# Kernel optimization log

Hardware: AMD Instinct MI355X
Metric: run time of the kernel (lower is better)

Reference implementation:

```python
import jax, jax.numpy as jnp
import numpy as np

NUM_HEADS = 16
LN_EPS = 1e-5


def setup_inputs() -> dict:
    key = jax.random.key(0)
    k1, k2, k3 = jax.random.split(key, 3)
    E = 1024
    B, S = 4, 2048
    return {
        "rotation_params": jax.random.normal(k1, (E, E), dtype=jnp.float32) * (E ** -0.5),
        "entangle_params": jax.random.normal(k2, (E, E), dtype=jnp.float32) * (E ** -0.5),
        "inputs": jax.random.normal(k3, (B, S, E), dtype=jnp.float32),
        "ln_weight": jnp.ones((E,), dtype=jnp.float32),
        "ln_bias": jnp.zeros((E,), dtype=jnp.float32),
    }


def reference(rotation_params, entangle_params, inputs, ln_weight, ln_bias):
    x = inputs  # (B, S, E)
    B, S, E = x.shape
    H = NUM_HEADS
    D = E // H
    scale = D ** -0.5

    q = jnp.einsum('bse,ef->bsf', x, rotation_params)
    k = jnp.einsum('bse,ef->bsf', x, entangle_params)
    v = x  # forward uses raw inputs as values

    # split heads: (B, H, S, D)
    q = q.reshape(B, S, H, D).transpose(0, 2, 1, 3)
    k = k.reshape(B, S, H, D).transpose(0, 2, 1, 3)
    v = v.reshape(B, S, H, D).transpose(0, 2, 1, 3)

    scores = jnp.einsum('bhsd,bhtd->bhst', q, k) * scale  # (B, H, S, S)
    attn = jax.nn.softmax(scores, axis=-1)
    context = jnp.einsum('bhst,bhtd->bhsd', attn, v)
    context = context.transpose(0, 2, 1, 3).reshape(B, S, E)

    # residual + LayerNorm
    y = context + x
    mu = jnp.mean(y, axis=-1, keepdims=True)
    var = jnp.mean(jnp.square(y - mu), axis=-1, keepdims=True)
    y = (y - mu) * jax.lax.rsqrt(var + LN_EPS)
    return y * ln_weight + ln_bias
```

## Files before the change

kernel.cpp:

```cpp
#include <hip/hip_runtime.h>
#include <hip/hip_bf16.h>

#define LOG2E 1.44269504088896340736f

typedef __attribute__((ext_vector_type(8)))  short  short8;
typedef __attribute__((ext_vector_type(2)))  float  f32x2;
typedef __attribute__((ext_vector_type(4)))  float  f32x4;
typedef __attribute__((ext_vector_type(16))) float  f32x16;

__device__ __forceinline__ unsigned short f2bf(float f) {
  unsigned u = __builtin_bit_cast(unsigned, f);
  return (unsigned short)((u + 0x8000u) >> 16);
}
__device__ __forceinline__ float bf2f(unsigned short u) {
  return __builtin_bit_cast(float, (unsigned)u << 16);
}
__device__ __forceinline__ f32x2 pkadd(f32x2 a, f32x2 b) {
  f32x2 r; asm("v_pk_add_f32 %0, %1, %2" : "=v"(r) : "v"(a), "v"(b)); return r;
}
__device__ __forceinline__ unsigned cvtpk2(float a, float b) {
  unsigned r; asm("v_cvt_pk_bf16_f32 %0, %1, %2" : "=v"(r) : "v"(a), "v"(b)); return r;
}
__device__ __forceinline__ float hexp2(float x) {
  float r; asm("v_exp_f32 %0, %1" : "=v"(r) : "v"(x)); return r;
}
__device__ __forceinline__ float m3(float a, float b, float c) {
  return fmaxf(fmaxf(a, b), c);
}
__device__ __forceinline__ void gl16(const void* g, void* l) {
  __builtin_amdgcn_global_load_lds(
      (const __attribute__((address_space(1))) void*)g,
      (__attribute__((address_space(3))) void*)l, 16, 0, 0);
}

__global__ __launch_bounds__(256) void prep_all(const float* __restrict__ R,
                                                const float* __restrict__ En,
                                                const float* __restrict__ x,
                                                unsigned short* __restrict__ Rt,
                                                unsigned short* __restrict__ Et,
                                                unsigned short* __restrict__ vt,
                                                unsigned short* __restrict__ xb) {
  int id = blockIdx.x;
  int tid = threadIdx.x;
  __shared__ unsigned short t[64][65];
  if (id < 2048) {
    int bh = id >> 5, st = id & 31;
    int b = bh >> 4, h = bh & 15;
    int s0 = st * 64;
#pragma unroll
    for (int i = 0; i < 4; i++) {
      int it = i * 256 + tid;
      int row = it >> 4, c4 = (it & 15) * 4;
      size_t goff = (size_t)(b * 2048 + s0 + row) * 1024 + h * 64 + c4;
      float4 v = *(const float4*)(x + goff);
      ushort4 o;
      o.x = f2bf(v.x); o.y = f2bf(v.y); o.z = f2bf(v.z); o.w = f2bf(v.w);
      *(ushort4*)(xb + goff) = o;
      t[c4 + 0][row] = o.x; t[c4 + 1][row] = o.y;
      t[c4 + 2][row] = o.z; t[c4 + 3][row] = o.w;
    }
    __syncthreads();
    int r = tid >> 2, c4 = (tid & 3) * 16;
    short8 o0, o1;
#pragma unroll
    for (int j = 0; j < 8; j++) {
      o0[j] = (short)t[r][c4 + j];
      o1[j] = (short)t[r][c4 + 8 + j];
    }
    *(short8*)(vt + (size_t)(bh * 64 + r) * 2048 + s0 + c4) = o0;
    *(short8*)(vt + (size_t)(bh * 64 + r) * 2048 + s0 + c4 + 8) = o1;
  } else {
    int z = id - 2048;
    const float* src = (z >= 256) ? En : R;
    unsigned short* dst = (z >= 256) ? Et : Rt;
    int rem = z & 255;
    int e0 = (rem >> 4) * 64, f0 = (rem & 15) * 64;
    int r = tid >> 2, c4 = (tid & 3) * 16;
#pragma unroll
    for (int j = 0; j < 16; j += 4) {
      float4 v = *(const float4*)(src + (size_t)(e0 + r) * 1024 + f0 + c4 + j);
      t[c4 + j + 0][r] = f2bf(v.x);
      t[c4 + j + 1][r] = f2bf(v.y);
      t[c4 + j + 2][r] = f2bf(v.z);
      t[c4 + j + 3][r] = f2bf(v.w);
    }
    __syncthreads();
    short8 o0, o1;
#pragma unroll
    for (int j = 0; j < 8; j++) {
      o0[j] = (short)t[r][c4 + j];
      o1[j] = (short)t[r][c4 + 8 + j];
    }
    *(short8*)(dst + (size_t)(f0 + r) * 1024 + e0 + c4) = o0;
    *(short8*)(dst + (size_t)(f0 + r) * 1024 + e0 + c4 + 8) = o1;
  }
}

__global__ __launch_bounds__(512, 2) void gemm8(const unsigned short* __restrict__ A,
                                                const unsigned short* __restrict__ Bw,
                                                unsigned short* __restrict__ qb,
                                                unsigned short* __restrict__ kb,
                                                float qs) {
  int m0 = blockIdx.x * 256;
  int by = blockIdx.y;
  int n0 = by * 256;
  int tid = threadIdx.x;
  int w = tid >> 6, l = tid & 63;
  int wr = w >> 2, wc = w & 3;
  int l15 = l & 15, lq = l >> 4;

  __shared__ unsigned short As[2][2][128 * 64];
  __shared__ unsigned short Bs[2][2][128 * 64];

  f32x4 acc[8][4] = {};

  int key = (l15 & 7) << 4;
  const char* pA[2];
  const char* pB[2];
#pragma unroll
  for (int kk = 0; kk < 2; kk++) {
    pA[kk] = (const char*)As + wr * 16384 + l15 * 128 + ((kk * 64 + lq * 16) ^ key);
    pB[kk] = (const char*)Bs + (wc >> 1) * 16384 + ((wc & 1) * 64 + l15) * 128 +
             ((kk * 64 + lq * 16) ^ key);
  }

#define SHALF(buf, kt, which)                                                 \
  do {                                                                        \
    const unsigned short* src_ = ((which) < 2)                                \
        ? (A  + (size_t)(m0 + ((which) & 1) * 128) * 1024)                    \
        : (Bw + (size_t)(n0 + ((which) & 1) * 128) * 1024);                   \
    char* dst_ = (char*)(((which) < 2) ? &As[buf][(which) & 1][0]             \
                                       : &Bs[buf][(which) & 1][0]);           \
    int k0_ = (kt) * 64;                                                      \
    _Pragma("unroll") for (int i_ = 0; i_ < 2; i_++) {                        \
      int flat_ = i_ * 512 + tid;                                             \
      int row_ = flat_ >> 3, ch_ = flat_ & 7;                                 \
      gl16(src_ + (size_t)row_ * 1024 + k0_ + ((ch_ ^ (row_ & 7)) << 3),      \
           dst_ + i_ * 8192 + w * 1024);                                      \
    }                                                                         \
  } while (0)

#define BARX()                                                                \
  do {                                                                        \
    __builtin_amdgcn_sched_barrier(0);                                        \
    asm volatile("" ::: "memory");                                            \
    __builtin_amdgcn_s_barrier();                                             \
    asm volatile("" ::: "memory");                                            \
    __builtin_amdgcn_sched_barrier(0);                                        \
  } while (0)

#define DSRD(buf, mq, nq)                                                     \
  short8 af[4][2]; short8 bfv[2][2];                                          \
  _Pragma("unroll") for (int mfq = 0; mfq < 4; mfq++)                         \
    _Pragma("unroll") for (int kk = 0; kk < 2; kk++)                          \
      af[mfq][kk] = *(const short8*)(pA[kk] + (buf) * 32768 + (mq) * 8192 +   \
                                     mfq * 2048);                             \
  _Pragma("unroll") for (int nfq = 0; nfq < 2; nfq++)                         \
    _Pragma("unroll") for (int kk = 0; kk < 2; kk++)                          \
      bfv[nfq][kk] = *(const short8*)(pB[kk] + (buf) * 32768 + (nq) * 4096 +  \
                                      nfq * 2048);

#define MM(mq, nq)                                                            \
  asm volatile("s_waitcnt lgkmcnt(0)" ::: "memory");                          \
  __builtin_amdgcn_sched_barrier(0);                                          \
  __builtin_amdgcn_s_setprio(1);                                              \
  _Pragma("unroll") for (int mfq = 0; mfq < 4; mfq++)                         \
    _Pragma("unroll") for (int nfq = 0; nfq < 2; nfq++)                       \
      _Pragma("unroll") for (int kk = 0; kk < 2; kk++)                        \
        acc[(mq) * 4 + mfq][(nq) * 2 + nfq] =                                 \
            __builtin_amdgcn_mfma_f32_16x16x32_bf16(                          \
                af[mfq][kk], bfv[nfq][kk],                                    \
                acc[(mq) * 4 + mfq][(nq) * 2 + nfq], 0, 0, 0);                \
  __builtin_amdgcn_s_setprio(0);

  SHALF(0, 0, 0); SHALF(0, 0, 1); SHALF(0, 0, 2); SHALF(0, 0, 3);
  asm volatile("s_waitcnt vmcnt(0)" ::: "memory");
  BARX();

  for (int kt = 0; kt < 16; kt++) {
    int buf = kt & 1, nb = buf ^ 1;
    {
      DSRD(buf, 0, 0);
      if (kt < 15) { SHALF(nb, kt + 1, 0); SHALF(nb, kt + 1, 1); }
      MM(0, 0);
      BARX();
    }
    {
      DSRD(buf, 0, 1);
      if (kt < 15) { SHALF(nb, kt + 1, 2); SHALF(nb, kt + 1, 3); }
      MM(0, 1);
      BARX();
    }
    {
      DSRD(buf, 1, 0);
      MM(1, 0);
      BARX();
    }
    {
      DSRD(buf, 1, 1);
      MM(1, 1);
      asm volatile("s_waitcnt vmcnt(0)" ::: "memory");
      BARX();
    }
  }
#undef SHALF
#undef DSRD
#undef MM
#undef BARX

  unsigned short* out = (by < 4) ? qb : kb;
  float scale = (by < 4) ? qs : 1.0f;
  int cb = (by & 3) * 256;
#pragma unroll
  for (int mf = 0; mf < 8; mf++)
#pragma unroll
    for (int nf = 0; nf < 4; nf++)
#pragma unroll
      for (int r = 0; r < 4; r++) {
        int grow = m0 + wr * 128 + mf * 16 + lq * 4 + r;
        int gcol = cb + wc * 64 + nf * 16 + l15;
        out[(size_t)grow * 1024 + gcol] = f2bf(acc[mf][nf][r] * scale);
      }
}

__global__ __launch_bounds__(256, 4) void attn_k(const unsigned short* __restrict__ Q,
                                                 const unsigned short* __restrict__ K,
                                                 const unsigned short* __restrict__ VT,
                                                 unsigned short* __restrict__ ctx) {
  int f = blockIdx.x;
  int bh = ((f >> 7) << 3) | (f & 7);
  int qt = (f >> 3) & 15;
  int b = bh >> 4, h = bh & 15;
  int q0 = qt * 128;
  int tid = threadIdx.x;
  int w = tid >> 6, l = tid & 63;
  int lh = l >> 5, l31 = l & 31;

  __shared__ unsigned short Kl[2 * 64 * 64];
  __shared__ unsigned short Vl[2 * 64 * 64];

  int qrow = q0 + w * 32 + l31;
  const unsigned short* qp = Q + (size_t)(b * 2048 + qrow) * 1024 + h * 64;
  short8 qf[4];
#pragma unroll
  for (int dk = 0; dk < 4; dk++) qf[dk] = *(const short8*)(qp + dk * 16 + lh * 8);

  int key = (l31 & 7) << 4;
  int koff[4], voff[4];
#pragma unroll
  for (int dk = 0; dk < 4; dk++) koff[dk] = l31 * 128 + ((dk * 32 + lh * 16) ^ key);
#pragma unroll
  for (int tf = 0; tf < 2; tf++)
#pragma unroll
    for (int kk = 0; kk < 2; kk++)
      voff[tf * 2 + kk] = l31 * 128 + ((tf * 64 + kk * 32 + lh * 16) ^ key);

  const char* KB = (const char*)Kl;
  const char* VB = (const char*)Vl;

  f32x16 cacc[2] = {};
  float mrun = -INFINITY, lsl = 0.f;

#define STAGE(buf, tt)                                                        \
  {                                                                           \
    _Pragma("unroll") for (int i_ = 0; i_ < 2; i_++) {                        \
      int row_ = i_ * 32 + (tid >> 3), ch_ = tid & 7;                         \
      gl16(K + (size_t)(b * 2048 + (tt) + row_) * 1024 + h * 64 +             \
               ((ch_ ^ (row_ & 7)) << 3),                                     \
           (char*)Kl + (buf) * 8192 + i_ * 4096 + w * 1024);                  \
      gl16(VT + (size_t)(bh * 64 + row_) * 2048 + (tt) +                      \
               ((ch_ ^ (row_ & 7)) << 3),                                     \
           (char*)Vl + (buf) * 8192 + i_ * 4096 + w * 1024);                  \
    }                                                                         \
  }

#define COMPUTE(IMM)                                                          \
  do {                                                                        \
    f32x16 sacc[2] = {};                                                      \
    __builtin_amdgcn_s_setprio(1);                                            \
    _Pragma("unroll") for (int tf = 0; tf < 2; tf++)                          \
      _Pragma("unroll") for (int dk = 0; dk < 4; dk++) {                      \
        short8 kf = *(const short8*)(KB + koff[dk] + (IMM) + tf * 4096);      \
        sacc[tf] = __builtin_amdgcn_mfma_f32_32x32x16_bf16(kf, qf[dk],        \
                                                           sacc[tf], 0, 0, 0);\
      }                                                                       \
    __builtin_amdgcn_s_setprio(0);                                            \
    float t16[16];                                                            \
    _Pragma("unroll") for (int j = 0; j < 16; j++)                            \
      t16[j] = fmaxf(sacc[0][j], sacc[1][j]);                                 \
    float t8[8];                                                              \
    _Pragma("unroll") for (int j = 0; j < 8; j++)                             \
      t8[j] = fmaxf(t16[j], t16[j + 8]);                                      \
    float lmax = m3(m3(t8[0], t8[1], t8[2]), m3(t8[3], t8[4], t8[5]),         \
                    fmaxf(t8[6], t8[7]));                                     \
    if (!__all(lmax <= mrun + 8.f)) {                                         \
      unsigned lu = __builtin_bit_cast(unsigned, lmax);                       \
      auto rr = __builtin_amdgcn_permlane32_swap(lu, lu, false, false);       \
      float pm = fmaxf(__builtin_bit_cast(float, rr[0]),                      \
                       __builtin_bit_cast(float, rr[1]));                     \
      float mnew = fmaxf(mrun, pm);                                           \
      float alpha = hexp2(mrun - mnew);                                       \
      mrun = mnew; lsl *= alpha;                                              \
      _Pragma("unroll") for (int r = 0; r < 16; r++) {                        \
        int rowq = (r & 3) + ((r >> 2) << 3) + (lh << 2);                     \
        float ar = __shfl(alpha, rowq, 64);                                   \
        cacc[0][r] *= ar; cacc[1][r] *= ar;                                   \
      }                                                                       \
    }                                                                         \
    f32x2 negm2; negm2[0] = -mrun; negm2[1] = -mrun;                          \
    f32x2 r2; r2[0] = 0.f; r2[1] = 0.f;                                       \
    _Pragma("unroll") for (int tf = 0; tf < 2; tf++) {                        \
      unsigned pw[8];                                                         \
      _Pragma("unroll") for (int j = 0; j < 8; j++) {                         \
        f32x2 s2; s2[0] = sacc[tf][2 * j]; s2[1] = sacc[tf][2 * j + 1];       \
        f32x2 d = pkadd(s2, negm2);                                           \
        float e0 = hexp2(d[0]), e1 = hexp2(d[1]);                             \
        f32x2 e2; e2[0] = e0; e2[1] = e1;                                     \
        r2 = pkadd(r2, e2);                                                   \
        pw[j] = cvtpk2(e0, e1);                                               \
      }                                                                       \
      short8 pa[2];                                                           \
      _Pragma("unroll") for (int kk = 0; kk < 2; kk++) {                      \
        auto r02 = __builtin_amdgcn_permlane32_swap(pw[kk * 4 + 0],           \
                                                    pw[kk * 4 + 2], false, false); \
        auto r13 = __builtin_amdgcn_permlane32_swap(pw[kk * 4 + 1],           \
                                                    pw[kk * 4 + 3], false, false); \
        union { unsigned u[4]; short8 s8; } wv;                               \
        wv.u[0] = r02[0]; wv.u[1] = r13[0];                                   \
        wv.u[2] = r02[1]; wv.u[3] = r13[1];                                   \
        pa[kk] = wv.s8;                                                       \
      }                                                                       \
      __builtin_amdgcn_s_setprio(1);                                          \
      _Pragma("unroll") for (int kk = 0; kk < 2; kk++)                        \
        _Pragma("unroll") for (int df = 0; df < 2; df++) {                    \
          short8 vf = *(const short8*)(VB + voff[tf * 2 + kk] + (IMM) +       \
                                       df * 4096);                            \
          cacc[df] = __builtin_amdgcn_mfma_f32_32x32x16_bf16(pa[kk], vf,      \
                                                             cacc[df], 0, 0, 0); \
        }                                                                     \
      __builtin_amdgcn_s_setprio(0);                                          \
    }                                                                         \
    lsl += r2[0] + r2[1];                                                     \
  } while (0)

  STAGE(0, 0);
  __syncthreads();

  for (int tc2 = 0; tc2 < 16; tc2++) {
    int t0 = tc2 * 128;
    STAGE(1, t0 + 64);
    COMPUTE(0);
    __syncthreads();
    if (tc2 < 15) STAGE(0, t0 + 128);
    COMPUTE(8192);
    __syncthreads();
  }
#undef STAGE
#undef COMPUTE

  {
    unsigned lu = __builtin_bit_cast(unsigned, lsl);
    auto rr = __builtin_amdgcn_permlane32_swap(lu, lu, false, false);
    lsl = __builtin_bit_cast(float, rr[0]) + __builtin_bit_cast(float, rr[1]);
  }
  float linv = 1.f / lsl;
#pragma unroll
  for (int r = 0; r < 16; r++) {
    int rowq = (r & 3) + ((r >> 2) << 3) + (lh << 2);
    float lr = __shfl(linv, rowq, 64);
    size_t base = (size_t)(b * 2048 + q0 + w * 32 + rowq) * 1024 + h * 64 + l31;
    ctx[base]      = f2bf(cacc[0][r] * lr);
    ctx[base + 32] = f2bf(cacc[1][r] * lr);
  }
}

__global__ __launch_bounds__(256) void ln_k(const unsigned short* __restrict__ ctx,
                                            const float* __restrict__ x,
                                            const float* __restrict__ wgt,
                                            const float* __restrict__ bgam,
                                            float* __restrict__ out) {
  int w = threadIdx.x >> 6, l = threadIdx.x & 63;
  size_t base = ((size_t)blockIdx.x * 4 + w) * 1024;
  float y[16];
  float s = 0.f, ss = 0.f;
#pragma unroll
  for (int j = 0; j < 4; j++) {
    int col = j * 256 + l * 4;
    ushort4 cu = *(const ushort4*)(ctx + base + col);
    float4 xv = *(const float4*)(x + base + col);
    float y0 = bf2f(cu.x) + xv.x, y1 = bf2f(cu.y) + xv.y;
    float y2 = bf2f(cu.z) + xv.z, y3 = bf2f(cu.w) + xv.w;
    y[4 * j + 0] = y0; y[4 * j + 1] = y1; y[4 * j + 2] = y2; y[4 * j + 3] = y3;
    s += (y0 + y1) + (y2 + y3);
    ss += (y0 * y0 + y1 * y1) + (y2 * y2 + y3 * y3);
  }
#pragma unroll
  for (int o = 32; o >= 1; o >>= 1) {
    s  += __shfl_xor(s, o, 64);
    ss += __shfl_xor(ss, o, 64);
  }
  float mu = s * (1.f / 1024.f);
  float var = ss * (1.f / 1024.f) - mu * mu;
  float rstd = rsqrtf(var + 1e-5f);
#pragma unroll
  for (int j = 0; j < 4; j++) {
    int col = j * 256 + l * 4;
    float4 wv = *(const float4*)(wgt + col);
    float4 bv = *(const float4*)(bgam + col);
    float4 o4;
    o4.x = (y[4 * j + 0] - mu) * rstd * wv.x + bv.x;
    o4.y = (y[4 * j + 1] - mu) * rstd * wv.y + bv.y;
    o4.z = (y[4 * j + 2] - mu) * rstd * wv.z + bv.z;
    o4.w = (y[4 * j + 3] - mu) * rstd * wv.w + bv.w;
    *(float4*)(out + base + col) = o4;
  }
}

extern "C" void kernel_launch(void* const* d_in, const int* in_sizes, int n_in,
                              void* d_out, int out_size, void* d_ws, size_t ws_size,
                              hipStream_t stream) {
  (void)in_sizes; (void)n_in; (void)out_size; (void)ws_size;
  const float* R  = (const float*)d_in[0];
  const float* En = (const float*)d_in[1];
  const float* x  = (const float*)d_in[2];
  const float* lw = (const float*)d_in[3];
  const float* lb = (const float*)d_in[4];
  float* out = (float*)d_out;

  char* ws = (char*)d_ws;
  unsigned short* xb  = (unsigned short*)(ws);
  unsigned short* qb  = (unsigned short*)(ws + (size_t)(16u << 20));
  unsigned short* kb  = (unsigned short*)(ws + (size_t)(32u << 20));
  unsigned short* vt  = (unsigned short*)(ws + (size_t)(48u << 20));
  unsigned short* ctx = (unsigned short*)(ws + (size_t)(64u << 20));
  unsigned short* rt  = (unsigned short*)(ws + (size_t)(96u << 20));
  unsigned short* et  = (unsigned short*)(ws + (size_t)(98u << 20));

  prep_all<<<2560, 256, 0, stream>>>(R, En, x, rt, et, vt, xb);
  gemm8<<<dim3(32, 8), 512, 0, stream>>>(xb, rt, qb, kb, 0.125f * LOG2E);
  attn_k<<<1024, 256, 0, stream>>>(qb, kb, vt, ctx);
  ln_k<<<2048, 256, 0, stream>>>(ctx, x, lw, lb, out);
}
```

Before: 243.5 us.

## Split attention key range in two and merge partials in LayerNorm kernel

The attention kernel now splits the 2048-key sequence into two halves handled by separate blocks, doubling the grid to 2048 blocks. Each block writes a normalized partial context plus its running max and sum, and the LayerNorm kernel merges the two partials with log-sum-exp weights before the residual add. This targets low occupancy and tail effects from 1024 long-running blocks on the MI355X's compute units. In exchange it adds extra partial-output traffic, a second bf16 rounding of the partials, and merge arithmetic in the LayerNorm pass.

```diff
diff --git a/kernel.cpp b/kernel.cpp
--- a/kernel.cpp
+++ b/kernel.cpp
@@ -226,12 +226,16 @@
 __global__ __launch_bounds__(256, 4) void attn_k(const unsigned short* __restrict__ Q,
                                                  const unsigned short* __restrict__ K,
                                                  const unsigned short* __restrict__ VT,
-                                                 unsigned short* __restrict__ ctx) {
+                                                 unsigned short* __restrict__ opart,
+                                                 float2* __restrict__ mlb) {
   int f = blockIdx.x;
-  int bh = ((f >> 7) << 3) | (f & 7);
-  int qt = (f >> 3) & 15;
+  int sp = f >> 10;
+  int g = f & 1023;
+  int bh = ((g >> 7) << 3) | (g & 7);
+  int qt = (g >> 3) & 15;
   int b = bh >> 4, h = bh & 15;
   int q0 = qt * 128;
+  int tbase = sp << 10;
   int tid = threadIdx.x;
   int w = tid >> 6, l = tid & 63;
   int lh = l >> 5, l31 = l & 31;
@@ -343,15 +347,15 @@
     lsl += r2[0] + r2[1];                                                     \
   } while (0)
 
-  STAGE(0, 0);
+  STAGE(0, tbase);
   __syncthreads();
 
-  for (int tc2 = 0; tc2 < 16; tc2++) {
-    int t0 = tc2 * 128;
+  for (int tc2 = 0; tc2 < 8; tc2++) {
+    int t0 = tbase + tc2 * 128;
     STAGE(1, t0 + 64);
     COMPUTE(0);
     __syncthreads();
-    if (tc2 < 15) STAGE(0, t0 + 128);
+    if (tc2 < 7) STAGE(0, t0 + 128);
     COMPUTE(8192);
     __syncthreads();
   }
@@ -364,42 +368,62 @@
     lsl = __builtin_bit_cast(float, rr[0]) + __builtin_bit_cast(float, rr[1]);
   }
   float linv = 1.f / lsl;
+  unsigned short* op = opart + (size_t)sp * (8u << 20);
 #pragma unroll
   for (int r = 0; r < 16; r++) {
     int rowq = (r & 3) + ((r >> 2) << 3) + (lh << 2);
     float lr = __shfl(linv, rowq, 64);
     size_t base = (size_t)(b * 2048 + q0 + w * 32 + rowq) * 1024 + h * 64 + l31;
-    ctx[base]      = f2bf(cacc[0][r] * lr);
-    ctx[base + 32] = f2bf(cacc[1][r] * lr);
-  }
-}
-
-__global__ __launch_bounds__(256) void ln_k(const unsigned short* __restrict__ ctx,
+    op[base]      = f2bf(cacc[0][r] * lr);
+    op[base + 32] = f2bf(cacc[1][r] * lr);
+  }
+  if (lh == 0) {
+    float2 ml; ml.x = mrun; ml.y = lsl;
+    mlb[(size_t)sp * 131072 + (size_t)bh * 2048 + qrow] = ml;
+  }
+}
+
+__global__ __launch_bounds__(256) void ln_k(const unsigned short* __restrict__ opart,
+                                            const float2* __restrict__ mlb,
                                             const float* __restrict__ x,
                                             const float* __restrict__ wgt,
                                             const float* __restrict__ bgam,
                                             float* __restrict__ out) {
   int w = threadIdx.x >> 6, l = threadIdx.x & 63;
-  size_t base = ((size_t)blockIdx.x * 4 + w) * 1024;
+  int row = blockIdx.x * 4 + w;
+  int b = row >> 11, s = row & 2047;
+  size_t base = (size_t)row * 1024;
+  const unsigned short* o2p = opart + (8u << 20);
   float y[16];
-  float s = 0.f, ss = 0.f;
+  float sum = 0.f, ss = 0.f;
 #pragma unroll
   for (int j = 0; j < 4; j++) {
     int col = j * 256 + l * 4;
-    ushort4 cu = *(const ushort4*)(ctx + base + col);
+    int h = j * 4 + (l >> 4);
+    float2 ml1 = mlb[(size_t)(b * 16 + h) * 2048 + s];
+    float2 ml2 = mlb[131072 + (size_t)(b * 16 + h) * 2048 + s];
+    float mm = fmaxf(ml1.x, ml2.x);
+    float w1 = ml1.y * hexp2(ml1.x - mm);
+    float w2 = ml2.y * hexp2(ml2.x - mm);
+    float inv = 1.f / (w1 + w2);
+    float a1 = w1 * inv, a2 = w2 * inv;
+    ushort4 c1 = *(const ushort4*)(opart + base + col);
+    ushort4 c2 = *(const ushort4*)(o2p + base + col);
     float4 xv = *(const float4*)(x + base + col);
-    float y0 = bf2f(cu.x) + xv.x, y1 = bf2f(cu.y) + xv.y;
-    float y2 = bf2f(cu.z) + xv.z, y3 = bf2f(cu.w) + xv.w;
+    float y0 = a1 * bf2f(c1.x) + a2 * bf2f(c2.x) + xv.x;
+    float y1 = a1 * bf2f(c1.y) + a2 * bf2f(c2.y) + xv.y;
+    float y2 = a1 * bf2f(c1.z) + a2 * bf2f(c2.z) + xv.z;
+    float y3 = a1 * bf2f(c1.w) + a2 * bf2f(c2.w) + xv.w;
     y[4 * j + 0] = y0; y[4 * j + 1] = y1; y[4 * j + 2] = y2; y[4 * j + 3] = y3;
-    s += (y0 + y1) + (y2 + y3);
+    sum += (y0 + y1) + (y2 + y3);
     ss += (y0 * y0 + y1 * y1) + (y2 * y2 + y3 * y3);
   }
 #pragma unroll
   for (int o = 32; o >= 1; o >>= 1) {
-    s  += __shfl_xor(s, o, 64);
-    ss += __shfl_xor(ss, o, 64);
-  }
-  float mu = s * (1.f / 1024.f);
+    sum += __shfl_xor(sum, o, 64);
+    ss  += __shfl_xor(ss, o, 64);
+  }
+  float mu = sum * (1.f / 1024.f);
   float var = ss * (1.f / 1024.f) - mu * mu;
   float rstd = rsqrtf(var + 1e-5f);
 #pragma unroll
@@ -432,12 +456,13 @@
   unsigned short* qb  = (unsigned short*)(ws + (size_t)(16u << 20));
   unsigned short* kb  = (unsigned short*)(ws + (size_t)(32u << 20));
   unsigned short* vt  = (unsigned short*)(ws + (size_t)(48u << 20));
-  unsigned short* ctx = (unsigned short*)(ws + (size_t)(64u << 20));
+  unsigned short* op  = (unsigned short*)(ws + (size_t)(64u << 20));
   unsigned short* rt  = (unsigned short*)(ws + (size_t)(96u << 20));
   unsigned short* et  = (unsigned short*)(ws + (size_t)(98u << 20));
+  float2*         mlb = (float2*)(ws + (size_t)(100u << 20));
 
   prep_all<<<2560, 256, 0, stream>>>(R, En, x, rt, et, vt, xb);
   gemm8<<<dim3(32, 8), 512, 0, stream>>>(xb, rt, qb, kb, 0.125f * LOG2E);
-  attn_k<<<1024, 256, 0, stream>>>(qb, kb, vt, ctx);
-  ln_k<<<2048, 256, 0, stream>>>(ctx, x, lw, lb, out);
-}
+  attn_k<<<2048, 256, 0, stream>>>(qb, kb, vt, op, mlb);
+  ln_k<<<2048, 256, 0, stream>>>(op, mlb, x, lw, lb, out);
+}
```

Result: no change. 244.3 us (+0.3%).
